# Kernel tuning notes

Measured on AMD Instinct MI355X. Metric: run time of the kernel, lower is better.

Reference implementation:

```python
import jax, jax.numpy as jnp
import numpy as np

GROUP_MANTISSA = 8
GROUP_SIZE = 36


def bfp_quantize(x, mantissa=GROUP_MANTISSA, group_size=GROUP_SIZE):
    """Block floating point: flatten, group consecutive group_size elements,
    share the max exponent within each group, keep `mantissa` mantissa bits."""
    flat = x.reshape(-1)
    n = flat.shape[0]
    pad = (-n) % group_size
    f = jnp.pad(flat, (0, pad)).reshape(-1, group_size)  # [G, group_size]
    m = jnp.max(jnp.abs(f), axis=1, keepdims=True)       # group max magnitude
    safe_m = jnp.where(m > 0, m, jnp.ones_like(m))
    e = jnp.floor(jnp.log2(safe_m))                      # shared exponent
    scale = jnp.exp2(e - (mantissa - 1))                 # LSB step for the group
    q = jnp.round(f / scale) * scale
    q = jnp.where(m > 0, q, jnp.zeros_like(q))
    return q.reshape(-1)[:n].reshape(x.shape)


def setup_inputs() -> dict:
    key = jax.random.key(0)
    kx, kw, kb = jax.random.split(key, 3)
    x = jax.random.normal(kx, (32, 64, 112, 112), dtype=jnp.float32)
    # kaiming-uniform-ish scale for a 3x3x64 fan-in
    fan_in = 64 * 3 * 3
    bound = 1.0 / np.sqrt(fan_in)
    weight = jax.random.uniform(kw, (64, 64, 3, 3), dtype=jnp.float32, minval=-bound, maxval=bound) * np.sqrt(3.0)
    bias = jax.random.uniform(kb, (64,), dtype=jnp.float32, minval=-bound, maxval=bound)
    return {"x": x, "weight": weight, "bias": bias}


def reference(x, weight, bias):
    xq = bfp_quantize(x)
    wq = bfp_quantize(weight)
    out = jax.lax.conv_general_dilated(
        xq, wq,
        window_strides=(1, 1),
        padding=((1, 1), (1, 1)),
        lhs_dilation=(1, 1),
        rhs_dilation=(1, 1),
        dimension_numbers=("NCHW", "OIHW", "NCHW"),
        feature_group_count=1,
    )
    return out + bias[None, :, None, None]
```

## Files before the change

kernel.cpp:

```cpp
#include <hip/hip_runtime.h>

typedef __attribute__((ext_vector_type(4))) float f32x4;
typedef __attribute__((ext_vector_type(8))) short s16x8;
typedef __attribute__((ext_vector_type(2))) unsigned int u32x2;
typedef __attribute__((ext_vector_type(4))) unsigned int u32x4;

#define X_ELEMS 25690112
#define X_F4    6422528
#define HW 112
#define PW 120
#define PPLANE (112*120)
#define CHW (64*112*112)

__device__ __forceinline__ unsigned short f32_to_bf16_exact(float q) {
    return (unsigned short)(__float_as_uint(q) >> 16);
}

__device__ __forceinline__ unsigned int pack_bf16x2(float a, float b) {
    return __builtin_amdgcn_perm(__float_as_uint(b), __float_as_uint(a), 0x07060302u);
}

__device__ __forceinline__ void scale_from_max(float m, float& scale, float& inv) {
    if (m > 0.f) {
        int e = (int)((__float_as_uint(m) >> 23) & 0xFF) - 127;
        scale = __builtin_ldexpf(1.0f, e - 7);
        inv   = __builtin_ldexpf(1.0f, 7 - e);
    } else { scale = 0.f; inv = 0.f; }
}

__global__ __launch_bounds__(256) void q1_quant(const float* __restrict__ x,
                                                const float* __restrict__ w,
                                                unsigned short* __restrict__ xq,
                                                unsigned short* __restrict__ wt) {
    __shared__ float lmax[2304];
    __shared__ float lsc[256];
    __shared__ float linv[256];
    const int b = blockIdx.x, tid = threadIdx.x;

    if (b == 2788) {
        #pragma unroll 1
        for (int rep = 0; rep < 4; ++rep) {
            int g = rep * 256 + tid;
            const float4* p = (const float4*)w + g * 9;
            float vv[36]; float m = 0.f;
            #pragma unroll
            for (int i = 0; i < 9; ++i) {
                float4 v = p[i];
                vv[i*4+0]=v.x; vv[i*4+1]=v.y; vv[i*4+2]=v.z; vv[i*4+3]=v.w;
                m = fmaxf(m, fmaxf(fmaxf(fabsf(v.x), fabsf(v.y)), fmaxf(fabsf(v.z), fabsf(v.w))));
            }
            float s, inv; scale_from_max(m, s, inv);
            #pragma unroll
            for (int j = 0; j < 36; ++j) {
                int flat = g * 36 + j;
                int k = flat / 576, rem = flat % 576;
                int c = rem / 9, pp = rem % 9;
                float q = rintf(vv[j] * inv) * s;
                wt[pp * 4096 + k * 64 + c] = f32_to_bf16_exact(q);
            }
        }
        return;
    }

    long base4 = (long)b * 2304;
    float4 vv[9];
    #pragma unroll
    for (int it = 0; it < 9; ++it) {
        int i = it * 256 + tid;
        long g4 = base4 + i;
        float4 v = {0.f, 0.f, 0.f, 0.f};
        if (g4 < X_F4) v = ((const float4*)x)[g4];
        vv[it] = v;
        lmax[i] = fmaxf(fmaxf(fabsf(v.x), fabsf(v.y)), fmaxf(fabsf(v.z), fabsf(v.w)));
    }
    __syncthreads();
    {
        float m = 0.f; int o = tid * 9;
        #pragma unroll
        for (int j = 0; j < 9; ++j) m = fmaxf(m, lmax[o + j]);
        float s, inv; scale_from_max(m, s, inv);
        lsc[tid] = s; linv[tid] = inv;
    }
    __syncthreads();
    #pragma unroll
    for (int it = 0; it < 9; ++it) {
        int i = it * 256 + tid;
        int g4 = (int)base4 + i;
        if (g4 < X_F4) {
            int lg = i / 9;
            float s = lsc[lg], inv = linv[lg];
            float4 v = vv[it];
            u32x2 o;
            o.x = pack_bf16x2(rintf(v.x * inv) * s, rintf(v.y * inv) * s);
            o.y = pack_bf16x2(rintf(v.z * inv) * s, rintf(v.w * inv) * s);
            int flat = g4 * 4;
            int plane = flat / 12544;
            int rw = flat - plane * 12544;
            int h = rw / 112, ww = rw - h * 112;
            int rowb = plane * PPLANE + h * PW;
            *(u32x2*)(xq + rowb + 4 + ww) = o;
            if (ww == 0)        *(u32x2*)(xq + rowb) = (u32x2){0u, 0u};
            else if (ww == 108) *(u32x2*)(xq + rowb + 116) = (u32x2){0u, 0u};
        }
    }
}

__device__ __forceinline__ int swz(int pix, int oct) {
    return pix * 72 + (((oct) ^ ((pix >> 3) & 7)) << 3);
}

__global__ __launch_bounds__(256, 2) void conv_mfma(const unsigned short* __restrict__ xq,
                                                    const unsigned short* __restrict__ wt,
                                                    const float* __restrict__ bias,
                                                    float* __restrict__ out) {
    __shared__ unsigned short xs[360 * 72];
    const int tid = threadIdx.x;
    const int wave = tid >> 6, lane = tid & 63;
    const int wl = lane & 15, quad = lane >> 4;
    const int kg = wave & 1, mg = wave >> 1;
    int b = blockIdx.x;
    b = (b & 7) * 224 + (b >> 3);
    const int n = b / 56, rem = b % 56;
    const int h0 = (rem >> 2) * 8, w0 = (rem & 3) * 28;

    #pragma unroll
    for (int tt = 0; tt < 2; ++tt) {
        int t = tt * 256 + tid;
        if (t < 320) {
            int oct = t / 40;
            int rm = t - oct * 40;
            int r = rm >> 2, wq = rm & 3;
            int hh = h0 - 1 + r;
            int c0 = w0 + 2 + wq * 8;
            u32x4 v[8];
            if (hh >= 0 && hh < HW) {
                const unsigned short* src = xq + (n * 64 + oct * 8) * PPLANE + hh * PW + c0;
                #pragma unroll
                for (int j = 0; j < 8; ++j)
                    v[j] = *(const u32x4*)(src + j * PPLANE);
            } else {
                #pragma unroll
                for (int j = 0; j < 8; ++j) v[j] = (u32x4){0u, 0u, 0u, 0u};
            }
            int pix0 = r * 36 + wq * 8 + 2;
            #pragma unroll
            for (int d = 0; d < 8; ++d) {
                unsigned int sel = (d & 1) ? 0x07060302u : 0x05040100u;
                int k = d >> 1;
                u32x4 o;
                o.x = __builtin_amdgcn_perm(v[1][k], v[0][k], sel);
                o.y = __builtin_amdgcn_perm(v[3][k], v[2][k], sel);
                o.z = __builtin_amdgcn_perm(v[5][k], v[4][k], sel);
                o.w = __builtin_amdgcn_perm(v[7][k], v[6][k], sel);
                *(u32x4*)&xs[swz(pix0 + d, oct)] = o;
            }
        }
    }

    s16x8 Bf[9][2][2];
    #pragma unroll
    for (int p = 0; p < 9; ++p)
        #pragma unroll
        for (int cs = 0; cs < 2; ++cs)
            #pragma unroll
            for (int j = 0; j < 2; ++j)
                Bf[p][cs][j] = *(const s16x8*)(wt + p * 4096 +
                                ((kg * 2 + j) * 16 + wl) * 64 + cs * 32 + quad * 8);

    float bv[2];
    #pragma unroll
    for (int j = 0; j < 2; ++j) bv[j] = bias[kg * 32 + j * 16 + wl];

    int pixb[7];
    #pragma unroll
    for (int mti = 0; mti < 7; ++mti) {
        int m = (mg * 7 + mti) * 16 + wl;
        pixb[mti] = (m / 28) * 36 + (m % 28) + 3;
    }

    __syncthreads();

    f32x4 acc[7][2];
    f32x4 zero = {0.f, 0.f, 0.f, 0.f};
    #pragma unroll
    for (int mti = 0; mti < 7; ++mti) { acc[mti][0] = zero; acc[mti][1] = zero; }

    #pragma unroll
    for (int p = 0; p < 9; ++p) {
        const int dpix = (p / 3) * 36 + (p % 3);
        #pragma unroll
        for (int cs = 0; cs < 2; ++cs) {
            s16x8 A[7];
            #pragma unroll
            for (int mti = 0; mti < 7; ++mti)
                A[mti] = *(const s16x8*)&xs[swz(pixb[mti] + dpix, cs * 4 + quad)];
            #pragma unroll
            for (int mti = 0; mti < 7; ++mti) {
                acc[mti][0] = __builtin_amdgcn_mfma_f32_16x16x32_bf16(A[mti], Bf[p][cs][0], acc[mti][0], 0, 0, 0);
                acc[mti][1] = __builtin_amdgcn_mfma_f32_16x16x32_bf16(A[mti], Bf[p][cs][1], acc[mti][1], 0, 0, 0);
            }
        }
    }

    int obase = n * CHW + h0 * HW + w0;
    #pragma unroll
    for (int mti = 0; mti < 7; ++mti) {
        int m0 = (mg * 7 + mti) * 16 + quad * 4;
        int eofs = (m0 / 28) * HW + (m0 % 28);
        #pragma unroll
        for (int j = 0; j < 2; ++j) {
            f32x4 v = acc[mti][j];
            v.x += bv[j]; v.y += bv[j]; v.z += bv[j]; v.w += bv[j];
            *(f32x4*)(out + obase + (kg * 32 + j * 16 + wl) * 12544 + eofs) = v;
        }
    }
}

extern "C" void kernel_launch(void* const* d_in, const int* in_sizes, int n_in,
                              void* d_out, int out_size, void* d_ws, size_t ws_size,
                              hipStream_t stream) {
    const float* x    = (const float*)d_in[0];
    const float* w    = (const float*)d_in[1];
    const float* bias = (const float*)d_in[2];
    float* out = (float*)d_out;
    char* ws = (char*)d_ws;
    unsigned short* xq = (unsigned short*)ws;
    unsigned short* wt = (unsigned short*)(ws + 55050240);

    hipLaunchKernelGGL(q1_quant,  dim3(2789), dim3(256), 0, stream, x, w, xq, wt);
    hipLaunchKernelGGL(conv_mfma, dim3(1792), dim3(256), 0, stream, xq, wt, bias, out);
}
```

Before: 259.6 us.

## Make conv kernel persistent with register-prefetched next tile overlapping MFMA

Changes the conv kernel from one tile per block (1792 blocks) to a persistent grid of 512 blocks, each looping over 3-4 tiles. Weights, bias and pixel offsets are loaded once per block and reused across tiles, and the next tile's input is prefetched into registers during the current tile's MFMA work, then written to LDS between barriers. This aims to hide global load latency and cut per-block setup cost. In exchange it raises register pressure from holding the prefetch buffers, which may hurt occupancy at 2 blocks/CU. It also leaves a tail imbalance, since the first 256 blocks do 4 tiles and the rest do 3.

```diff
diff --git a/kernel.cpp b/kernel.cpp
--- a/kernel.cpp
+++ b/kernel.cpp
@@ -109,6 +109,47 @@
     return pix * 72 + (((oct) ^ ((pix >> 3) & 7)) << 3);
 }
 
+__device__ __forceinline__ void tile_decode(int st, int& n, int& h0, int& w0) {
+    n = st / 56; int rem = st - n * 56;
+    h0 = (rem >> 2) * 8; w0 = (rem & 3) * 28;
+}
+
+__device__ __forceinline__ void regload_task(const unsigned short* __restrict__ xq,
+                                             int n, int h0, int w0, int t, u32x4 v[8]) {
+    int oct = t / 40;
+    int rm = t - oct * 40;
+    int r = rm >> 2, wq = rm & 3;
+    int hh = h0 - 1 + r;
+    int c0 = w0 + 2 + wq * 8;
+    if (hh >= 0 && hh < HW) {
+        const unsigned short* src = xq + (n * 64 + oct * 8) * PPLANE + hh * PW + c0;
+        #pragma unroll
+        for (int j = 0; j < 8; ++j)
+            v[j] = *(const u32x4*)(src + j * PPLANE);
+    } else {
+        #pragma unroll
+        for (int j = 0; j < 8; ++j) v[j] = (u32x4){0u, 0u, 0u, 0u};
+    }
+}
+
+__device__ __forceinline__ void permwrite_task(unsigned short* xs, int t, u32x4 v[8]) {
+    int oct = t / 40;
+    int rm = t - oct * 40;
+    int r = rm >> 2, wq = rm & 3;
+    int pix0 = r * 36 + wq * 8 + 2;
+    #pragma unroll
+    for (int d = 0; d < 8; ++d) {
+        unsigned int sel = (d & 1) ? 0x07060302u : 0x05040100u;
+        int k = d >> 1;
+        u32x4 o;
+        o.x = __builtin_amdgcn_perm(v[1][k], v[0][k], sel);
+        o.y = __builtin_amdgcn_perm(v[3][k], v[2][k], sel);
+        o.z = __builtin_amdgcn_perm(v[5][k], v[4][k], sel);
+        o.w = __builtin_amdgcn_perm(v[7][k], v[6][k], sel);
+        *(u32x4*)&xs[swz(pix0 + d, oct)] = o;
+    }
+}
+
 __global__ __launch_bounds__(256, 2) void conv_mfma(const unsigned short* __restrict__ xq,
                                                     const unsigned short* __restrict__ wt,
                                                     const float* __restrict__ bias,
@@ -118,44 +159,9 @@
     const int wave = tid >> 6, lane = tid & 63;
     const int wl = lane & 15, quad = lane >> 4;
     const int kg = wave & 1, mg = wave >> 1;
-    int b = blockIdx.x;
-    b = (b & 7) * 224 + (b >> 3);
-    const int n = b / 56, rem = b % 56;
-    const int h0 = (rem >> 2) * 8, w0 = (rem & 3) * 28;
-
-    #pragma unroll
-    for (int tt = 0; tt < 2; ++tt) {
-        int t = tt * 256 + tid;
-        if (t < 320) {
-            int oct = t / 40;
-            int rm = t - oct * 40;
-            int r = rm >> 2, wq = rm & 3;
-            int hh = h0 - 1 + r;
-            int c0 = w0 + 2 + wq * 8;
-            u32x4 v[8];
-            if (hh >= 0 && hh < HW) {
-                const unsigned short* src = xq + (n * 64 + oct * 8) * PPLANE + hh * PW + c0;
-                #pragma unroll
-                for (int j = 0; j < 8; ++j)
-                    v[j] = *(const u32x4*)(src + j * PPLANE);
-            } else {
-                #pragma unroll
-                for (int j = 0; j < 8; ++j) v[j] = (u32x4){0u, 0u, 0u, 0u};
-            }
-            int pix0 = r * 36 + wq * 8 + 2;
-            #pragma unroll
-            for (int d = 0; d < 8; ++d) {
-                unsigned int sel = (d & 1) ? 0x07060302u : 0x05040100u;
-                int k = d >> 1;
-                u32x4 o;
-                o.x = __builtin_amdgcn_perm(v[1][k], v[0][k], sel);
-                o.y = __builtin_amdgcn_perm(v[3][k], v[2][k], sel);
-                o.z = __builtin_amdgcn_perm(v[5][k], v[4][k], sel);
-                o.w = __builtin_amdgcn_perm(v[7][k], v[6][k], sel);
-                *(u32x4*)&xs[swz(pix0 + d, oct)] = o;
-            }
-        }
-    }
+    const int bs = blockIdx.x;
+    const int nt = (bs < 256) ? 4 : 3;
+    const bool has1 = (tid < 64);
 
     s16x8 Bf[9][2][2];
     #pragma unroll
@@ -166,11 +172,9 @@
             for (int j = 0; j < 2; ++j)
                 Bf[p][cs][j] = *(const s16x8*)(wt + p * 4096 +
                                 ((kg * 2 + j) * 16 + wl) * 64 + cs * 32 + quad * 8);
-
     float bv[2];
     #pragma unroll
     for (int j = 0; j < 2; ++j) bv[j] = bias[kg * 32 + j * 16 + wl];
-
     int pixb[7];
     #pragma unroll
     for (int mti = 0; mti < 7; ++mti) {
@@ -178,40 +182,72 @@
         pixb[mti] = (m / 28) * 36 + (m % 28) + 3;
     }
 
+    u32x4 v0[8], v1[8];
+    {
+        int t0 = bs;
+        int st = ((t0 & 7) * 224) + (t0 >> 3);
+        int n, h0, w0; tile_decode(st, n, h0, w0);
+        regload_task(xq, n, h0, w0, tid, v0);
+        if (has1) regload_task(xq, n, h0, w0, 256 + tid, v1);
+        permwrite_task(xs, tid, v0);
+        if (has1) permwrite_task(xs, 256 + tid, v1);
+    }
     __syncthreads();
 
-    f32x4 acc[7][2];
-    f32x4 zero = {0.f, 0.f, 0.f, 0.f};
-    #pragma unroll
-    for (int mti = 0; mti < 7; ++mti) { acc[mti][0] = zero; acc[mti][1] = zero; }
-
-    #pragma unroll
-    for (int p = 0; p < 9; ++p) {
-        const int dpix = (p / 3) * 36 + (p % 3);
-        #pragma unroll
-        for (int cs = 0; cs < 2; ++cs) {
-            s16x8 A[7];
-            #pragma unroll
-            for (int mti = 0; mti < 7; ++mti)
-                A[mti] = *(const s16x8*)&xs[swz(pixb[mti] + dpix, cs * 4 + quad)];
-            #pragma unroll
-            for (int mti = 0; mti < 7; ++mti) {
-                acc[mti][0] = __builtin_amdgcn_mfma_f32_16x16x32_bf16(A[mti], Bf[p][cs][0], acc[mti][0], 0, 0, 0);
-                acc[mti][1] = __builtin_amdgcn_mfma_f32_16x16x32_bf16(A[mti], Bf[p][cs][1], acc[mti][1], 0, 0, 0);
-            }
-        }
-    }
-
-    int obase = n * CHW + h0 * HW + w0;
-    #pragma unroll
-    for (int mti = 0; mti < 7; ++mti) {
-        int m0 = (mg * 7 + mti) * 16 + quad * 4;
-        int eofs = (m0 / 28) * HW + (m0 % 28);
-        #pragma unroll
-        for (int j = 0; j < 2; ++j) {
-            f32x4 v = acc[mti][j];
-            v.x += bv[j]; v.y += bv[j]; v.z += bv[j]; v.w += bv[j];
-            *(f32x4*)(out + obase + (kg * 32 + j * 16 + wl) * 12544 + eofs) = v;
+    #pragma unroll 1
+    for (int i = 0; i < nt; ++i) {
+        int tc = (i < 3) ? (bs + 512 * i) : (1536 + bs);
+        int st = ((tc & 7) * 224) + (tc >> 3);
+        int n, h0, w0; tile_decode(st, n, h0, w0);
+
+        if (i + 1 < nt) {
+            int tn = (i + 1 < 3) ? (bs + 512 * (i + 1)) : (1536 + bs);
+            int stn = ((tn & 7) * 224) + (tn >> 3);
+            int nn, hn, wn; tile_decode(stn, nn, hn, wn);
+            regload_task(xq, nn, hn, wn, tid, v0);
+            if (has1) regload_task(xq, nn, hn, wn, 256 + tid, v1);
+        }
+
+        f32x4 acc[7][2];
+        f32x4 zero = {0.f, 0.f, 0.f, 0.f};
+        #pragma unroll
+        for (int mti = 0; mti < 7; ++mti) { acc[mti][0] = zero; acc[mti][1] = zero; }
+
+        #pragma unroll
+        for (int p = 0; p < 9; ++p) {
+            const int dpix = (p / 3) * 36 + (p % 3);
+            #pragma unroll
+            for (int cs = 0; cs < 2; ++cs) {
+                s16x8 A[7];
+                #pragma unroll
+                for (int mti = 0; mti < 7; ++mti)
+                    A[mti] = *(const s16x8*)&xs[swz(pixb[mti] + dpix, cs * 4 + quad)];
+                #pragma unroll
+                for (int mti = 0; mti < 7; ++mti) {
+                    acc[mti][0] = __builtin_amdgcn_mfma_f32_16x16x32_bf16(A[mti], Bf[p][cs][0], acc[mti][0], 0, 0, 0);
+                    acc[mti][1] = __builtin_amdgcn_mfma_f32_16x16x32_bf16(A[mti], Bf[p][cs][1], acc[mti][1], 0, 0, 0);
+                }
+            }
+        }
+
+        int obase = n * CHW + h0 * HW + w0;
+        #pragma unroll
+        for (int mti = 0; mti < 7; ++mti) {
+            int m0 = (mg * 7 + mti) * 16 + quad * 4;
+            int eofs = (m0 / 28) * HW + (m0 % 28);
+            #pragma unroll
+            for (int j = 0; j < 2; ++j) {
+                f32x4 v = acc[mti][j];
+                v.x += bv[j]; v.y += bv[j]; v.z += bv[j]; v.w += bv[j];
+                *(f32x4*)(out + obase + (kg * 32 + j * 16 + wl) * 12544 + eofs) = v;
+            }
+        }
+
+        if (i + 1 < nt) {
+            __syncthreads();
+            permwrite_task(xs, tid, v0);
+            if (has1) permwrite_task(xs, 256 + tid, v1);
+            __syncthreads();
         }
     }
 }
@@ -228,5 +264,5 @@
     unsigned short* wt = (unsigned short*)(ws + 55050240);
 
     hipLaunchKernelGGL(q1_quant,  dim3(2789), dim3(256), 0, stream, x, w, xq, wt);
-    hipLaunchKernelGGL(conv_mfma, dim3(1792), dim3(256), 0, stream, xq, wt, bias, out);
-}
+    hipLaunchKernelGGL(conv_mfma, dim3(512),  dim3(256), 0, stream, xq, wt, bias, out);
+}
```

New measurement: 430.6 us. 1.66x slower.
